# Optimization experiments

Hardware: AMD Instinct MI355X
Metric: run time of the kernel (lower is better)

Reference implementation:

```python
import jax, jax.numpy as jnp
import numpy as np

N = 4096
INPUT_DIM = 1024
H1 = 512
H2 = 256
NUM_CLASS = 16
ALPHA = 0.2  # leaky relu slope in GAT layers
NEG_INF = -9e15


def _xavier(key, shape, gain=1.414):
    fan_in, fan_out = shape[0], shape[1]
    bound = gain * np.sqrt(6.0 / (fan_in + fan_out))
    return jax.random.uniform(key, shape, jnp.float32, -bound, bound)


def setup_inputs() -> dict:
    key = jax.random.key(0)
    ks = jax.random.split(key, 16)
    X = jax.random.normal(ks[0], (N, INPUT_DIM), jnp.float32)
    Y = jax.random.normal(ks[1], (N, NUM_CLASS), jnp.float32)
    noise = jax.random.normal(ks[2], (N, H2), jnp.float32)
    adj = jax.random.bernoulli(ks[3], 32.0 / N, (N, N))  # bool mask, avg degree ~32
    # GAT layer params: W [in,out], a [2*out,1]
    W0 = _xavier(ks[4], (INPUT_DIM, H1))
    a0 = _xavier(ks[5], (2 * H1, 1))
    W1 = _xavier(ks[6], (H1 + NUM_CLASS, H2))
    a1 = _xavier(ks[7], (2 * H2, 1))
    W2 = _xavier(ks[8], (H1 + NUM_CLASS, H2))
    a2 = _xavier(ks[9], (2 * H2, 1))
    # decoder MLP
    fc1_w = _xavier(ks[10], (H2 + NUM_CLASS, H1), gain=1.0)
    fc1_b = jnp.zeros((H1,), jnp.float32)
    fc2_w = _xavier(ks[11], (H1, N), gain=1.0)
    fc2_b = jnp.zeros((N,), jnp.float32)
    return {"X": X, "Y": Y, "noise": noise, "adj": adj,
            "W0": W0, "a0": a0, "W1": W1, "a1": a1, "W2": W2, "a2": a2,
            "fc1_w": fc1_w, "fc1_b": fc1_b, "fc2_w": fc2_w, "fc2_b": fc2_b}


def gat_layer(x, W, a, adj):
    # Faithful to the torch layer but without materializing [N*N, 2F]:
    # a_input @ a == (h @ a[:F]) broadcast-added to (h @ a[F:]).T
    h = x @ W                       # [N, F]
    F_ = W.shape[1]
    f_src = (h @ a[:F_]).squeeze(-1)  # [N] contribution of row node i
    f_dst = (h @ a[F_:]).squeeze(-1)  # [N] contribution of col node j
    e = jax.nn.leaky_relu(f_src[:, None] + f_dst[None, :], ALPHA)  # [N, N]
    e = jnp.where(adj, e, NEG_INF)
    att = jax.nn.softmax(e, axis=1)  # dropout prob is 0 in this model
    h_prime = att @ h               # [N, F]
    return jax.nn.elu(h_prime)      # concat=True default -> ELU


def reference(X, Y, noise, adj, W0, a0, W1, a1, W2, a2, fc1_w, fc1_b, fc2_w, fc2_b):
    hidden = gat_layer(X, W0, a0, adj)            # [N, H1]
    hidden = jnp.concatenate([hidden, Y], axis=1)  # [N, H1+C]
    mean = gat_layer(hidden, W1, a1, adj)          # [N, H2]
    logstd = gat_layer(hidden, W2, a2, adj)        # [N, H2]
    z = noise * jnp.exp(logstd) + mean             # reparameterization
    z = jnp.concatenate([z, Y], axis=1)            # [N, H2+C]
    z = jax.nn.relu(z @ fc1_w + fc1_b)             # [N, H1]
    A_pred = jax.nn.sigmoid(z @ fc2_w + fc2_b)     # [N, N]
    return A_pred
```

## Files before the change

### kernel.cpp

```cpp
#include <hip/hip_runtime.h>

#define LRELU_ALPHA 0.2f
#define NN 4096
#define CAP 256

typedef unsigned short u16;
typedef short bf16x8 __attribute__((ext_vector_type(8)));
typedef float f32x4 __attribute__((ext_vector_type(4)));
typedef u16 u16x4 __attribute__((ext_vector_type(4)));
typedef u16 u16x2 __attribute__((ext_vector_type(2)));
typedef u16 u16x8 __attribute__((ext_vector_type(8)));

__device__ __forceinline__ u16 f2bf(float f) {
  unsigned u = __float_as_uint(f);
  u += 0x7FFFu + ((u >> 16) & 1u);
  return (u16)(u >> 16);
}
__device__ __forceinline__ float bf2f(u16 u) {
  return __uint_as_float(((unsigned)u) << 16);
}

__device__ __forceinline__ float waveSum(float v) {
  #pragma unroll
  for (int o = 32; o > 0; o >>= 1) v += __shfl_xor(v, o, 64);
  return v;
}
__device__ __forceinline__ float waveMax(float v) {
  #pragma unroll
  for (int o = 32; o > 0; o >>= 1) v = fmaxf(v, __shfl_xor(v, o, 64));
  return v;
}

__device__ __forceinline__ void gload_lds16(const void* g, void* l) {
  __builtin_amdgcn_global_load_lds((const __attribute__((address_space(1))) void*)g,
                                   (__attribute__((address_space(3))) void*)l, 16, 0, 0);
}

__device__ __forceinline__ void lds_barrier() {
  asm volatile("s_waitcnt lgkmcnt(0)" ::: "memory");
  __builtin_amdgcn_s_barrier();
}

__device__ __forceinline__ void csr_body(const unsigned* __restrict__ adjw,
                                         int* __restrict__ nbr, int* __restrict__ cnt,
                                         int i, int* wsum)
{
  const int tid = threadIdx.x;
  const int w = tid >> 6, lane = tid & 63;
  unsigned bits = 0;
  const unsigned* row = adjw + (size_t)i * 4096 + tid * 16;
  #pragma unroll
  for (int ck = 0; ck < 4; ++ck) {
    uint4 v = *(const uint4*)(row + ck * 4);
    if (v.x) bits |= 1u << (ck * 4 + 0);
    if (v.y) bits |= 1u << (ck * 4 + 1);
    if (v.z) bits |= 1u << (ck * 4 + 2);
    if (v.w) bits |= 1u << (ck * 4 + 3);
  }
  int mycnt = __popc(bits);
  int incl = mycnt;
  #pragma unroll
  for (int o = 1; o < 64; o <<= 1) {
    int v = __shfl_up(incl, o, 64);
    if (lane >= o) incl += v;
  }
  if (lane == 63) wsum[w] = incl;
  __syncthreads();
  int base = 0;
  #pragma unroll
  for (int k = 0; k < 4; ++k) base += (k < w) ? wsum[k] : 0;
  const int total = wsum[0] + wsum[1] + wsum[2] + wsum[3];
  int pos = base + incl - mycnt;
  #pragma unroll
  for (int b = 0; b < 16; ++b) {
    if (bits & (1u << b)) {
      if (pos < CAP) nbr[(size_t)i * CAP + pos] = tid * 16 + b;
      ++pos;
    }
  }
  if (tid == 0) cnt[i] = total;
}

__device__ __forceinline__ void transpose_body(const float* Wsrc, u16* Wt,
                                               int K, int N, int Kpad,
                                               int bx, int by, float (*t)[33]) {
  const int kb = by * 32, nb = bx * 32;
  const int tx = threadIdx.x & 31, ty = threadIdx.x >> 5;
  for (int i = ty; i < 32; i += 8) {
    int k = kb + i, n = nb + tx;
    t[i][tx] = (k < K && n < N) ? Wsrc[(size_t)k * N + n] : 0.f;
  }
  __syncthreads();
  for (int i = ty; i < 32; i += 8) {
    int n = nb + i, k = kb + tx;
    if (n < N && k < Kpad) Wt[(size_t)n * Kpad + k] = f2bf(t[tx][i]);
  }
}

__global__ __launch_bounds__(256) void prep_all(
    const float* __restrict__ W0, u16* __restrict__ W0t,
    const float* __restrict__ W1, u16* __restrict__ W1t,
    const float* __restrict__ W2, u16* __restrict__ W2t,
    const float* __restrict__ fc1w, u16* __restrict__ fc1t,
    const float* __restrict__ X, u16* __restrict__ Xb,
    float* __restrict__ fsz)
{
  __shared__ float t[32][33];
  const int i = blockIdx.x, tid = threadIdx.x;
  if (i < 512) {
    transpose_body(W0, W0t, 1024, 512, 1024, i & 15, i >> 4, t);
  } else if (i < 656) {
    int j = i - 512;
    transpose_body(W1, W1t, 528, 256, 576, j & 7, j >> 3, t);
  } else if (i < 800) {
    int j = i - 656;
    transpose_body(W2, W2t, 528, 256, 576, j & 7, j >> 3, t);
  } else if (i < 960) {
    int j = i - 800;
    transpose_body(fc1w, fc1t, 272, 512, 320, j & 15, j >> 4, t);
  } else if (i < 5056) {
    int j = i - 960;
    int idx = j * 256 + tid;
    float4 v = ((const float4*)X)[idx];
    u16x4 o = {f2bf(v.x), f2bf(v.y), f2bf(v.z), f2bf(v.w)};
    ((u16x4*)Xb)[idx] = o;
  } else {
    int j = i - 5056;
    ((f32x4*)fsz)[j * 256 + tid] = f32x4{0.f, 0.f, 0.f, 0.f};
  }
}

template<int ACT, bool OBF, int FS>
__device__ __forceinline__ void gemm64_dev(
    const u16* __restrict__ A, int lda,
    const u16* __restrict__ Bt, int ldb,
    void* __restrict__ Cout, int ldc,
    int K, const float* __restrict__ bias,
    u16 (&As)[2][128 * 64], u16 (&Bs)[2][64 * 64], int bid,
    const float* aA, const float* aB,
    float* fsA, float* fdA, float* fsB, float* fdB)
{
  const int tid = threadIdx.x;
  const int lane = tid & 63, wv = tid >> 6;
  const int wm = wv >> 1, wn = wv & 1;
  const int swz = ((bid & 7) << 5) | (bid >> 3);
  const int m0 = (swz >> 3) * 128, n0 = (swz & 7) * 64;
  const int nk = K >> 6;

  f32x4 acc[4][2] = {};

  auto STAGE = [&](int buf, int kt) {
    #pragma unroll
    for (int i = 0; i < 4; ++i) {
      int c = tid + i * 256;
      int r = c >> 3, sl = c & 7;
      int sg = sl ^ (r & 7);
      gload_lds16(A + (size_t)(m0 + r) * lda + kt * 64 + sg * 8, (char*)As[buf] + (c & ~63) * 16);
    }
    #pragma unroll
    for (int i = 0; i < 2; ++i) {
      int c = tid + i * 256;
      int r = c >> 3, sl = c & 7;
      int sg = sl ^ (r & 7);
      gload_lds16(Bt + (size_t)(n0 + r) * ldb + kt * 64 + sg * 8, (char*)Bs[buf] + (c & ~63) * 16);
    }
  };

  STAGE(0, 0);
  if (nk > 1) STAGE(1, 1);

  int cur = 0;
  for (int kt = 0; kt < nk; ++kt) {
    if (kt + 1 < nk) { asm volatile("s_waitcnt vmcnt(6)" ::: "memory"); }
    else             { asm volatile("s_waitcnt vmcnt(0)" ::: "memory"); }
    __builtin_amdgcn_s_barrier();

    #pragma unroll
    for (int ks = 0; ks < 2; ++ks) {
      bf16x8 af[4], bf_[2];
      #pragma unroll
      for (int mi = 0; mi < 4; ++mi) {
        int r = wm * 64 + mi * 16 + (lane & 15);
        int sl = (ks * 4 + (lane >> 4)) ^ (r & 7);
        af[mi] = *(const bf16x8*)((const char*)As[cur] + r * 128 + sl * 16);
      }
      #pragma unroll
      for (int ni = 0; ni < 2; ++ni) {
        int r = wn * 32 + ni * 16 + (lane & 15);
        int sl = (ks * 4 + (lane >> 4)) ^ (r & 7);
        bf_[ni] = *(const bf16x8*)((const char*)Bs[cur] + r * 128 + sl * 16);
      }
      __builtin_amdgcn_s_setprio(1);
      #pragma unroll
      for (int mi = 0; mi < 4; ++mi)
        #pragma unroll
        for (int ni = 0; ni < 2; ++ni)
          acc[mi][ni] = __builtin_amdgcn_mfma_f32_16x16x32_bf16(af[mi], bf_[ni], acc[mi][ni], 0, 0, 0);
      __builtin_amdgcn_s_setprio(0);
    }

    __builtin_amdgcn_s_barrier();
    if (kt + 2 < nk) STAGE(cur, kt + 2);
    cur ^= 1;
  }

  float bv2[2];
  #pragma unroll
  for (int ni = 0; ni < 2; ++ni)
    bv2[ni] = bias ? bias[n0 + wn * 32 + ni * 16 + (lane & 15)] : 0.f;
  float* sc = (float*)As;
  #pragma unroll
  for (int mi = 0; mi < 4; ++mi) {
    lds_barrier();
    const int lr = wm * 16 + (lane >> 4) * 4;
    #pragma unroll
    for (int ni = 0; ni < 2; ++ni) {
      const int lc = wn * 32 + ni * 16 + (lane & 15);
      #pragma unroll
      for (int j = 0; j < 4; ++j) {
        float v = acc[mi][ni][j] + bv2[ni];
        if (ACT == 1) v = fmaxf(v, 0.f);
        if (ACT == 2) v = 1.f / (1.f + __expf(-v));
        sc[(lr + j) * 64 + lc] = v;
      }
    }
    lds_barrier();
    if constexpr (FS > 0) {
      const float* aS; const float* aD; float* fsO; float* fdO; int colbase;
      if constexpr (FS == 1) {
        aS = aA; aD = aA + 512; fsO = fsA; fdO = fdA; colbase = n0;
      } else {
        const bool lo2 = (n0 < 256);
        const float* av = lo2 ? aA : aB;
        aS = av; aD = av + 256;
        fsO = lo2 ? fsA : fsB; fdO = lo2 ? fdA : fdB;
        colbase = n0 & 255;
      }
      const int rr = tid >> 3, cg = tid & 7;
      float s0 = 0.f, s1 = 0.f;
      #pragma unroll
      for (int q = 0; q < 8; ++q) {
        float hv = sc[rr * 64 + cg * 8 + q];
        s0 = fmaf(hv, aS[colbase + cg * 8 + q], s0);
        s1 = fmaf(hv, aD[colbase + cg * 8 + q], s1);
      }
      #pragma unroll
      for (int o = 1; o < 8; o <<= 1) {
        s0 += __shfl_xor(s0, o, 64);
        s1 += __shfl_xor(s1, o, 64);
      }
      if (cg == 0) {
        int grow = m0 + (rr >> 4) * 64 + mi * 16 + (rr & 15);
        atomicAdd(fsO + grow, s0);
        atomicAdd(fdO + grow, s1);
      }
    }
    #pragma unroll
    for (int u = 0; u < 2; ++u) {
      int idx = tid + u * 256;
      int r = idx >> 4, c4 = (idx & 15) * 4;
      int grow = m0 + (r >> 4) * 64 + mi * 16 + (r & 15);
      float4 v4 = *(const float4*)(sc + r * 64 + c4);
      if (OBF) {
        u16x4 o = {f2bf(v4.x), f2bf(v4.y), f2bf(v4.z), f2bf(v4.w)};
        *(u16x4*)((u16*)Cout + (size_t)grow * ldc + n0 + c4) = o;
      } else {
        *(float4*)((float*)Cout + (size_t)grow * ldc + n0 + c4) = v4;
      }
    }
  }
}

template<int ACT, bool OBF, int FS>
__global__ __launch_bounds__(256) void gemm_mfma64(
    const u16* __restrict__ A, int lda, const u16* __restrict__ Bt, int ldb,
    void* __restrict__ Cout, int ldc, int K, const float* __restrict__ bias,
    const float* aA, const float* aB,
    float* fsA, float* fdA, float* fsB, float* fdB)
{
  __shared__ u16 As[2][128 * 64];
  __shared__ u16 Bs[2][64 * 64];
  gemm64_dev<ACT, OBF, FS>(A, lda, Bt, ldb, Cout, ldc, K, bias, As, Bs,
                           blockIdx.y * 8 + blockIdx.x, aA, aB, fsA, fdA, fsB, fdB);
}

__global__ __launch_bounds__(256) void csr_gemm0(
    const u16* __restrict__ Xb, const u16* __restrict__ W0t, u16* __restrict__ h0b,
    const unsigned* __restrict__ adjw,
    int* __restrict__ nbr, int* __restrict__ cnt,
    const float* __restrict__ fc2w, u16* __restrict__ fc2t,
    const float* __restrict__ a0, float* __restrict__ fs0, float* __restrict__ fd0)
{
  __shared__ u16 As[2][128 * 64];
  __shared__ u16 Bs[2][64 * 64];
  if (blockIdx.x < 256) {
    gemm64_dev<0, true, 1>(Xb, 1024, W0t, 1024, h0b, 512, 1024, nullptr, As, Bs, blockIdx.x,
                           a0, nullptr, fs0, fd0, nullptr, nullptr);
  } else if (blockIdx.x < 4352) {
    csr_body(adjw, nbr, cnt, blockIdx.x - 256, (int*)As);
  } else {
    int j = blockIdx.x - 4352;
    transpose_body(fc2w, fc2t, 512, 4096, 512, j & 127, j >> 7, (float(*)[33])As);
  }
}

__global__ __launch_bounds__(512, 2) void gemm_fc2_8p(
    const u16* __restrict__ A, int lda,
    const u16* __restrict__ Bt, int ldb,
    float* __restrict__ Cout, int ldc,
    int K, const float* __restrict__ bias)
{
  __shared__ u16 As[2][2][128 * 64];
  __shared__ u16 Bs[2][2][128 * 64];
  const int tid = threadIdx.x;
  const int lane = tid & 63, wv = tid >> 6;
  const int wm = wv >> 2, wn = wv & 3;
  const int bid = blockIdx.y * 16 + blockIdx.x;
  const int swz = ((bid & 7) << 5) | (bid >> 3);
  const int m0 = (swz >> 4) * 256, n0 = (swz & 15) * 256;
  const int nk = K >> 6;

  f32x4 acc[8][4] = {};

  auto stA = [&](int slot, int h, int t) {
    const u16* Ap = A + (size_t)(m0 + h * 128) * lda + t * 64;
    #pragma unroll
    for (int i = 0; i < 2; ++i) {
      int c = tid + i * 512;
      int r = c >> 3, sl = c & 7;
      int sg = sl ^ (r & 7);
      gload_lds16(Ap + (size_t)r * lda + sg * 8, (char*)&As[slot][h][0] + (c & ~63) * 16);
    }
  };
  auto stB = [&](int slot, int h, int t) {
    const u16* Bp = Bt + (size_t)(n0 + h * 128) * ldb + t * 64;
    #pragma unroll
    for (int i = 0; i < 2; ++i) {
      int c = tid + i * 512;
      int r = c >> 3, sl = c & 7;
      int sg = sl ^ (r & 7);
      gload_lds16(Bp + (size_t)r * ldb + sg * 8, (char*)&Bs[slot][h][0] + (c & ~63) * 16);
    }
  };

  bf16x8 afl[4][2], afh[4][2], bfl[2][2], bfh[2][2];
  auto rdAq = [&](int slot, int mi0, bf16x8 (&dst)[4][2]) {
    #pragma unroll
    for (int m = 0; m < 4; ++m)
      #pragma unroll
      for (int ks = 0; ks < 2; ++ks) {
        int r = (mi0 + m) * 16 + (lane & 15);
        int sl = (ks * 4 + (lane >> 4)) ^ (r & 7);
        dst[m][ks] = *(const bf16x8*)((const char*)&As[slot][wm][0] + r * 128 + sl * 16);
      }
  };
  auto rdBq = [&](int slot, int ni0, bf16x8 (&dst)[2][2]) {
    #pragma unroll
    for (int n = 0; n < 2; ++n)
      #pragma unroll
      for (int ks = 0; ks < 2; ++ks) {
        int r = (wn & 1) * 64 + (ni0 + n) * 16 + (lane & 15);
        int sl = (ks * 4 + (lane >> 4)) ^ (r & 7);
        dst[n][ks] = *(const bf16x8*)((const char*)&Bs[slot][wn >> 1][0] + r * 128 + sl * 16);
      }
  };
  auto quad = [&](int mi0, int ni0, bf16x8 (&af)[4][2], bf16x8 (&bf)[2][2]) {
    __builtin_amdgcn_s_setprio(1);
    #pragma unroll
    for (int m = 0; m < 4; ++m)
      #pragma unroll
      for (int n = 0; n < 2; ++n)
        #pragma unroll
        for (int ks = 0; ks < 2; ++ks)
          acc[mi0 + m][ni0 + n] =
              __builtin_amdgcn_mfma_f32_16x16x32_bf16(af[m][ks], bf[n][ks], acc[mi0 + m][ni0 + n], 0, 0, 0);
    __builtin_amdgcn_s_setprio(0);
  };
  #define BARX() __builtin_amdgcn_s_barrier()

  stA(0, 0, 0); stA(0, 1, 0); stB(0, 0, 0); stB(0, 1, 0);
  stA(1, 0, 1); stA(1, 1, 1);
  asm volatile("s_waitcnt vmcnt(4)" ::: "memory");
  BARX();

  for (int j = 0; j < nk; j += 2) {
    const bool s2 = (j + 2) < nk;
    rdAq(0, 0, afl); rdBq(0, 0, bfl);
    stB(1, 0, j + 1);
    BARX(); quad(0, 0, afl, bfl); BARX();
    rdAq(0, 4, afh);
    stB(1, 1, j + 1);
    BARX(); quad(4, 0, afh, bfl); BARX();
    rdBq(0, 2, bfh);
    if (s2) stA(0, 0, j + 2);
    BARX(); quad(0, 2, afl, bfh); BARX();
    if (s2) {
      stA(0, 1, j + 2);
      asm volatile("s_waitcnt vmcnt(4)" ::: "memory");
    } else {
      asm volatile("s_waitcnt vmcnt(0)" ::: "memory");
    }
    BARX(); quad(4, 2, afh, bfh); BARX();
    rdAq(1, 0, afl); rdBq(1, 0, bfl);
    if (s2) stB(0, 0, j + 2);
    BARX(); quad(0, 0, afl, bfl); BARX();
    rdAq(1, 4, afh);
    if (s2) stB(0, 1, j + 2);
    BARX(); quad(4, 0, afh, bfl); BARX();
    rdBq(1, 2, bfh);
    if (s2) stA(1, 0, j + 3);
    BARX(); quad(0, 2, afl, bfh); BARX();
    if (s2) {
      stA(1, 1, j + 3);
      asm volatile("s_waitcnt vmcnt(4)" ::: "memory");
    } else {
      asm volatile("s_waitcnt vmcnt(0)" ::: "memory");
    }
    BARX(); quad(4, 2, afh, bfh); BARX();
  }

  float bv4[4];
  #pragma unroll
  for (int ni = 0; ni < 4; ++ni)
    bv4[ni] = bias[n0 + wn * 64 + ni * 16 + (lane & 15)];
  float* sc = (float*)As;
  #pragma unroll
  for (int mi2 = 0; mi2 < 8; mi2 += 2) {
    lds_barrier();
    #pragma unroll
    for (int dm = 0; dm < 2; ++dm) {
      const int mi = mi2 + dm;
      const int lr = wm * 32 + dm * 16 + (lane >> 4) * 4;
      #pragma unroll
      for (int ni = 0; ni < 4; ++ni) {
        const int lc = wn * 64 + ni * 16 + (lane & 15);
        #pragma unroll
        for (int j = 0; j < 4; ++j) {
          float v = acc[mi][ni][j] + bv4[ni];
          v = 1.f / (1.f + __expf(-v));
          sc[(lr + j) * 256 + lc] = v;
        }
      }
    }
    lds_barrier();
    #pragma unroll
    for (int u = 0; u < 8; ++u) {
      int idx = tid + u * 512;
      int r = idx >> 6, c4 = (idx & 63) * 4;
      int grow = m0 + (r >> 5) * 128 + (mi2 + ((r >> 4) & 1)) * 16 + (r & 15);
      f32x4 v4 = *(const f32x4*)(sc + r * 256 + c4);
      __builtin_nontemporal_store(v4, (f32x4*)(Cout + (size_t)grow * ldc + n0 + c4));
    }
  }
}

__global__ __launch_bounds__(256) void agg_gat0(
    const u16* __restrict__ h,
    const float* __restrict__ fs, const float* __restrict__ fd,
    const int* __restrict__ nbr, const int* __restrict__ cnt,
    const float* __restrict__ Y, u16* __restrict__ hb)
{
  __shared__ float2 np[4][CAP];
  const int tid = threadIdx.x;
  const int w = tid >> 6, lane = tid & 63;
  const int r = blockIdx.x * 4 + w;
  int c = cnt[r]; if (c > CAP) c = CAP;
  float acc[8] = {};
  const u16* hp = h + lane * 8;

  if (c > 0) {
    const float fsi = fs[r];
    float e[4];
    int jj[4];
    #pragma unroll
    for (int k = 0; k < 4; ++k) {
      int n = lane + k * 64;
      e[k] = -3.0e38f;
      if (n < c) {
        jj[k] = nbr[(size_t)r * CAP + n];
        float v = fsi + fd[jj[k]];
        e[k] = v > 0.f ? v : LRELU_ALPHA * v;
      }
    }
    float m = waveMax(fmaxf(fmaxf(e[0], e[1]), fmaxf(e[2], e[3])));
    float p[4], ps = 0.f;
    #pragma unroll
    for (int k = 0; k < 4; ++k) {
      int n = lane + k * 64;
      p[k] = (n < c) ? __expf(e[k] - m) : 0.f;
      ps += p[k];
    }
    const float inv = 1.f / waveSum(ps);
    #pragma unroll
    for (int k = 0; k < 4; ++k) {
      int n = lane + k * 64;
      if (n < c) np[w][n] = float2{__int_as_float(jj[k]), p[k] * inv};
    }
    #pragma unroll 4
    for (int n = 0; n < c; ++n) {
      float2 e2 = np[w][n];
      int j = __float_as_int(e2.x);
      float pn = e2.y;
      u16x8 hv = *(const u16x8*)(hp + (size_t)j * 512);
      #pragma unroll
      for (int q = 0; q < 8; ++q) acc[q] = fmaf(pn, bf2f(hv[q]), acc[q]);
    }
  } else {
    for (int j = 0; j < NN; ++j) {
      u16x8 hv = *(const u16x8*)(hp + (size_t)j * 512);
      #pragma unroll
      for (int q = 0; q < 8; ++q) acc[q] += bf2f(hv[q]);
    }
    #pragma unroll
    for (int q = 0; q < 8; ++q) acc[q] *= (1.f / NN);
  }
  u16x8 o;
  #pragma unroll
  for (int q = 0; q < 8; ++q) {
    float v = acc[q] > 0.f ? acc[q] : expm1f(acc[q]);
    o[q] = f2bf(v);
  }
  u16* row = hb + (size_t)r * 576;
  *(u16x8*)(row + lane * 8) = o;
  if (lane < 4) {
    float4 yv = *(const float4*)(Y + (size_t)r * 16 + 4 * lane);
    *(u16x4*)(row + 512 + 4 * lane) = u16x4{f2bf(yv.x), f2bf(yv.y), f2bf(yv.z), f2bf(yv.w)};
  } else if (lane < 16) {
    *(u16x4*)(row + 528 + 4 * (lane - 4)) = u16x4{0, 0, 0, 0};
  }
}

__global__ __launch_bounds__(256) void agg_gat12(
    const u16* __restrict__ h12,
    const float* __restrict__ fs1, const float* __restrict__ fd1,
    const float* __restrict__ fs2, const float* __restrict__ fd2,
    const int* __restrict__ nbr, const int* __restrict__ cnt,
    const float* __restrict__ noise, const float* __restrict__ Y,
    u16* __restrict__ zcat)
{
  __shared__ float4 np[4][CAP];
  const int tid = threadIdx.x;
  const int w = tid >> 6, lane = tid & 63;
  const int r = blockIdx.x * 4 + w;
  int c = cnt[r]; if (c > CAP) c = CAP;
  float acc[8] = {};
  const u16* hp = h12 + lane * 8;

  if (c > 0) {
    const float f1 = fs1[r], f2 = fs2[r];
    float e1[4], e2[4];
    int jj[4];
    #pragma unroll
    for (int k = 0; k < 4; ++k) {
      int n = lane + k * 64;
      e1[k] = -3.0e38f; e2[k] = -3.0e38f;
      if (n < c) {
        jj[k] = nbr[(size_t)r * CAP + n];
        float v1 = f1 + fd1[jj[k]], v2 = f2 + fd2[jj[k]];
        e1[k] = v1 > 0.f ? v1 : LRELU_ALPHA * v1;
        e2[k] = v2 > 0.f ? v2 : LRELU_ALPHA * v2;
      }
    }
    float g1 = waveMax(fmaxf(fmaxf(e1[0], e1[1]), fmaxf(e1[2], e1[3])));
    float g2 = waveMax(fmaxf(fmaxf(e2[0], e2[1]), fmaxf(e2[2], e2[3])));
    float q1[4], q2[4], s1p = 0.f, s2p = 0.f;
    #pragma unroll
    for (int k = 0; k < 4; ++k) {
      int n = lane + k * 64;
      q1[k] = (n < c) ? __expf(e1[k] - g1) : 0.f;
      q2[k] = (n < c) ? __expf(e2[k] - g2) : 0.f;
      s1p += q1[k]; s2p += q2[k];
    }
    const float i1 = 1.f / waveSum(s1p);
    const float i2 = 1.f / waveSum(s2p);
    #pragma unroll
    for (int k = 0; k < 4; ++k) {
      int n = lane + k * 64;
      if (n < c) np[w][n] = float4{__int_as_float(jj[k]), q1[k] * i1, q2[k] * i2, 0.f};
    }
    const bool loHalf = (lane < 32);
    #pragma unroll 4
    for (int n = 0; n < c; ++n) {
      float4 e4 = np[w][n];
      int j = __float_as_int(e4.x);
      float pn = loHalf ? e4.y : e4.z;
      u16x8 hv = *(const u16x8*)(hp + (size_t)j * 512);
      #pragma unroll
      for (int q = 0; q < 8; ++q) acc[q] = fmaf(pn, bf2f(hv[q]), acc[q]);
    }
  } else {
    for (int j = 0; j < NN; ++j) {
      u16x8 hv = *(const u16x8*)(hp + (size_t)j * 512);
      #pragma unroll
      for (int q = 0; q < 8; ++q) acc[q] += bf2f(hv[q]);
    }
    #pragma unroll
    for (int q = 0; q < 8; ++q) acc[q] *= (1.f / NN);
  }
  float v[8];
  #pragma unroll
  for (int q = 0; q < 8; ++q) v[q] = acc[q] > 0.f ? acc[q] : expm1f(acc[q]);
  float lsd[8];
  #pragma unroll
  for (int q = 0; q < 8; ++q) lsd[q] = __shfl_xor(v[q], 32, 64);
  u16* row = zcat + (size_t)r * 320;
  if (lane < 32) {
    const float* nz = noise + (size_t)r * 256 + lane * 8;
    float4 na = *(const float4*)nz, nbv = *(const float4*)(nz + 4);
    float nzv[8] = {na.x, na.y, na.z, na.w, nbv.x, nbv.y, nbv.z, nbv.w};
    u16x8 o;
    #pragma unroll
    for (int q = 0; q < 8; ++q)
      o[q] = f2bf(fmaf(nzv[q], __expf(lsd[q]), v[q]));
    *(u16x8*)(row + lane * 8) = o;
  } else if (lane < 36) {
    float4 yv = *(const float4*)(Y + (size_t)r * 16 + 4 * (lane - 32));
    *(u16x4*)(row + 256 + 4 * (lane - 32)) = u16x4{f2bf(yv.x), f2bf(yv.y), f2bf(yv.z), f2bf(yv.w)};
  } else if (lane < 48) {
    *(u16x4*)(row + 272 + 4 * (lane - 36)) = u16x4{0, 0, 0, 0};
  }
}

extern "C" void kernel_launch(void* const* d_in, const int* in_sizes, int n_in,
                              void* d_out, int out_size, void* d_ws, size_t ws_size,
                              hipStream_t stream)
{
  const float* X     = (const float*)d_in[0];
  const float* Y     = (const float*)d_in[1];
  const float* noise = (const float*)d_in[2];
  const void*  adj   = d_in[3];
  const float* W0    = (const float*)d_in[4];
  const float* a0    = (const float*)d_in[5];
  const float* W1    = (const float*)d_in[6];
  const float* a1    = (const float*)d_in[7];
  const float* W2    = (const float*)d_in[8];
  const float* a2    = (const float*)d_in[9];
  const float* fc1w  = (const float*)d_in[10];
  const float* fc1b  = (const float*)d_in[11];
  const float* fc2w  = (const float*)d_in[12];
  const float* fc2b  = (const float*)d_in[13];
  float* out = (float*)d_out;
  char* W = (char*)d_ws;

  u16*   Xb    = (u16*)(W + 0);
  u16*   zcatb = (u16*)(W + 0);
  u16*   zzb   = (u16*)(W + 2621440);
  u16*   h0b   = (u16*)(W + 8388608);
  u16*   h12b  = (u16*)(W + 8388608);
  u16*   hb    = (u16*)(W + 12582912);
  u16*   W0t   = (u16*)(W + 17301504);
  u16*   W12t  = (u16*)(W + 18350080);
  u16*   fc1t  = (u16*)(W + 18939904);
  u16*   fc2t  = (u16*)(W + 19267584);
  int*   nbr   = (int*)(W + 23461888);
  int*   cnt   = (int*)(W + 27656192);
  float* fs0   = (float*)(W + 27672576);
  float* fd0   = fs0 + 4096;
  float* fs1   = fd0 + 4096;
  float* fd1   = fs1 + 4096;
  float* fs2   = fd1 + 4096;
  float* fd2   = fs2 + 4096;

  prep_all<<<5080, 256, 0, stream>>>(W0, W0t, W1, W12t, W2, W12t + 256 * 576,
                                     fc1w, fc1t, X, Xb, fs0);

  csr_gemm0<<<6400, 256, 0, stream>>>(Xb, W0t, h0b, (const unsigned*)adj, nbr, cnt,
                                      fc2w, fc2t, a0, fs0, fd0);

  agg_gat0<<<1024, 256, 0, stream>>>(h0b, fs0, fd0, nbr, cnt, Y, hb);

  gemm_mfma64<0, true, 2><<<dim3(8, 32), 256, 0, stream>>>(
      hb, 576, W12t, 576, h12b, 512, 576, nullptr, a1, a2, fs1, fd1, fs2, fd2);

  agg_gat12<<<1024, 256, 0, stream>>>(h12b, fs1, fd1, fs2, fd2, nbr, cnt, noise, Y, zcatb);

  gemm_mfma64<1, true, 0><<<dim3(8, 32), 256, 0, stream>>>(
      zcatb, 320, fc1t, 320, zzb, 512, 320, fc1b,
      nullptr, nullptr, nullptr, nullptr, nullptr, nullptr);

  gemm_fc2_8p<<<dim3(16, 16), 512, 0, stream>>>(zzb, 512, fc2t, 512, out, 4096, 512, fc2b);
}
```

Measured before the change: 111.1 us.

## Fuse CSR neighbor-list build into first GAT aggregation kernel

Moves the adjacency-to-CSR conversion out of the combined gemm0 launch and into agg_gat0. Each wave now scans its own 4096-word adjacency row, does a wave-level prefix sum, and writes neighbor ids straight into LDS as well as to global nbr/cnt for later layers. The fc2 transpose blocks now handle two tiles each to shrink that grid. The aim is to avoid a global round trip for the neighbor list and to shorten the gemm0 launch. The cost is that the adjacency scan now sits serially in front of the aggregation inside agg_gat0 instead of overlapping with the GEMM blocks.

```diff
diff --git a/kernel.cpp b/kernel.cpp
--- a/kernel.cpp
+++ b/kernel.cpp
@@ -40,45 +40,8 @@
   asm volatile("s_waitcnt lgkmcnt(0)" ::: "memory");
   __builtin_amdgcn_s_barrier();
 }
-
-__device__ __forceinline__ void csr_body(const unsigned* __restrict__ adjw,
-                                         int* __restrict__ nbr, int* __restrict__ cnt,
-                                         int i, int* wsum)
-{
-  const int tid = threadIdx.x;
-  const int w = tid >> 6, lane = tid & 63;
-  unsigned bits = 0;
-  const unsigned* row = adjw + (size_t)i * 4096 + tid * 16;
-  #pragma unroll
-  for (int ck = 0; ck < 4; ++ck) {
-    uint4 v = *(const uint4*)(row + ck * 4);
-    if (v.x) bits |= 1u << (ck * 4 + 0);
-    if (v.y) bits |= 1u << (ck * 4 + 1);
-    if (v.z) bits |= 1u << (ck * 4 + 2);
-    if (v.w) bits |= 1u << (ck * 4 + 3);
-  }
-  int mycnt = __popc(bits);
-  int incl = mycnt;
-  #pragma unroll
-  for (int o = 1; o < 64; o <<= 1) {
-    int v = __shfl_up(incl, o, 64);
-    if (lane >= o) incl += v;
-  }
-  if (lane == 63) wsum[w] = incl;
-  __syncthreads();
-  int base = 0;
-  #pragma unroll
-  for (int k = 0; k < 4; ++k) base += (k < w) ? wsum[k] : 0;
-  const int total = wsum[0] + wsum[1] + wsum[2] + wsum[3];
-  int pos = base + incl - mycnt;
-  #pragma unroll
-  for (int b = 0; b < 16; ++b) {
-    if (bits & (1u << b)) {
-      if (pos < CAP) nbr[(size_t)i * CAP + pos] = tid * 16 + b;
-      ++pos;
-    }
-  }
-  if (tid == 0) cnt[i] = total;
+__device__ __forceinline__ void wave_lds_fence() {
+  asm volatile("s_waitcnt lgkmcnt(0)" ::: "memory");
 }
 
 __device__ __forceinline__ void transpose_body(const float* Wsrc, u16* Wt,
@@ -284,10 +247,8 @@
                            blockIdx.y * 8 + blockIdx.x, aA, aB, fsA, fdA, fsB, fdB);
 }
 
-__global__ __launch_bounds__(256) void csr_gemm0(
+__global__ __launch_bounds__(256) void gemm0_fc2t(
     const u16* __restrict__ Xb, const u16* __restrict__ W0t, u16* __restrict__ h0b,
-    const unsigned* __restrict__ adjw,
-    int* __restrict__ nbr, int* __restrict__ cnt,
     const float* __restrict__ fc2w, u16* __restrict__ fc2t,
     const float* __restrict__ a0, float* __restrict__ fs0, float* __restrict__ fd0)
 {
@@ -296,11 +257,14 @@
   if (blockIdx.x < 256) {
     gemm64_dev<0, true, 1>(Xb, 1024, W0t, 1024, h0b, 512, 1024, nullptr, As, Bs, blockIdx.x,
                            a0, nullptr, fs0, fd0, nullptr, nullptr);
-  } else if (blockIdx.x < 4352) {
-    csr_body(adjw, nbr, cnt, blockIdx.x - 256, (int*)As);
   } else {
-    int j = blockIdx.x - 4352;
-    transpose_body(fc2w, fc2t, 512, 4096, 512, j & 127, j >> 7, (float(*)[33])As);
+    int j = blockIdx.x - 256;
+    float(*t)[33] = (float(*)[33])As;
+    int t0 = j * 2;
+    transpose_body(fc2w, fc2t, 512, 4096, 512, t0 & 127, t0 >> 7, t);
+    __syncthreads();
+    int t1 = t0 + 1;
+    transpose_body(fc2w, fc2t, 512, 4096, 512, t1 & 127, t1 >> 7, t);
   }
 }
 
@@ -455,18 +419,54 @@
 }
 
 __global__ __launch_bounds__(256) void agg_gat0(
+    const unsigned* __restrict__ adjw,
     const u16* __restrict__ h,
     const float* __restrict__ fs, const float* __restrict__ fd,
-    const int* __restrict__ nbr, const int* __restrict__ cnt,
+    int* __restrict__ nbr, int* __restrict__ cnt,
     const float* __restrict__ Y, u16* __restrict__ hb)
 {
   __shared__ float2 np[4][CAP];
   const int tid = threadIdx.x;
   const int w = tid >> 6, lane = tid & 63;
   const int r = blockIdx.x * 4 + w;
-  int c = cnt[r]; if (c > CAP) c = CAP;
   float acc[8] = {};
   const u16* hp = h + lane * 8;
+
+  unsigned long long bits = 0;
+  const uint4* rp = (const uint4*)(adjw + (size_t)r * 4096) + lane * 16;
+  #pragma unroll
+  for (int ck = 0; ck < 16; ++ck) {
+    uint4 v = rp[ck];
+    if (v.x) bits |= 1ull << (ck * 4 + 0);
+    if (v.y) bits |= 1ull << (ck * 4 + 1);
+    if (v.z) bits |= 1ull << (ck * 4 + 2);
+    if (v.w) bits |= 1ull << (ck * 4 + 3);
+  }
+  int mycnt = __popcll(bits);
+  int incl = mycnt;
+  #pragma unroll
+  for (int o = 1; o < 64; o <<= 1) {
+    int v = __shfl_up(incl, o, 64);
+    if (lane >= o) incl += v;
+  }
+  const int total = __shfl(incl, 63, 64);
+  int c = total > CAP ? CAP : total;
+  {
+    int pos = incl - mycnt;
+    unsigned long long bb = bits;
+    while (bb) {
+      int b = __builtin_ctzll(bb);
+      bb &= bb - 1;
+      if (pos < CAP) {
+        int id = lane * 64 + b;
+        np[w][pos].x = __int_as_float(id);
+        nbr[(size_t)r * CAP + pos] = id;
+      }
+      ++pos;
+    }
+    if (lane == 0) cnt[r] = total;
+  }
+  wave_lds_fence();
 
   if (c > 0) {
     const float fsi = fs[r];
@@ -477,7 +477,7 @@
       int n = lane + k * 64;
       e[k] = -3.0e38f;
       if (n < c) {
-        jj[k] = nbr[(size_t)r * CAP + n];
+        jj[k] = __float_as_int(np[w][n].x);
         float v = fsi + fd[jj[k]];
         e[k] = v > 0.f ? v : LRELU_ALPHA * v;
       }
@@ -494,8 +494,9 @@
     #pragma unroll
     for (int k = 0; k < 4; ++k) {
       int n = lane + k * 64;
-      if (n < c) np[w][n] = float2{__int_as_float(jj[k]), p[k] * inv};
-    }
+      if (n < c) np[w][n].y = p[k] * inv;
+    }
+    wave_lds_fence();
     #pragma unroll 4
     for (int n = 0; n < c; ++n) {
       float2 e2 = np[w][n];
@@ -578,6 +579,7 @@
       int n = lane + k * 64;
       if (n < c) np[w][n] = float4{__int_as_float(jj[k]), q1[k] * i1, q2[k] * i2, 0.f};
     }
+    wave_lds_fence();
     const bool loHalf = (lane < 32);
     #pragma unroll 4
     for (int n = 0; n < c; ++n) {
@@ -664,10 +666,9 @@
   prep_all<<<5080, 256, 0, stream>>>(W0, W0t, W1, W12t, W2, W12t + 256 * 576,
                                      fc1w, fc1t, X, Xb, fs0);
 
-  csr_gemm0<<<6400, 256, 0, stream>>>(Xb, W0t, h0b, (const unsigned*)adj, nbr, cnt,
-                                      fc2w, fc2t, a0, fs0, fd0);
-
-  agg_gat0<<<1024, 256, 0, stream>>>(h0b, fs0, fd0, nbr, cnt, Y, hb);
+  gemm0_fc2t<<<1280, 256, 0, stream>>>(Xb, W0t, h0b, fc2w, fc2t, a0, fs0, fd0);
+
+  agg_gat0<<<1024, 256, 0, stream>>>((const unsigned*)adj, h0b, fs0, fd0, nbr, cnt, Y, hb);
 
   gemm_mfma64<0, true, 2><<<dim3(8, 32), 256, 0, stream>>>(
       hb, 576, W12t, 576, h12b, 512, 576, nullptr, a1, a2, fs1, fd1, fs2, fd2);
```

After: 114.6 us. 3.2% more time.
